# Optimization experiments

Hardware: AMD Instinct MI355X
Metric: run time of the kernel (lower is better)

## Reference

```python
import jax, jax.numpy as jnp
import numpy as np

EPS = 1e-5

def layer_norm(x, g, b):
    mu = jnp.mean(x, axis=-1, keepdims=True)
    var = jnp.mean(jnp.square(x - mu), axis=-1, keepdims=True)
    return (x - mu) * jax.lax.rsqrt(var + EPS) * g + b

def setup_inputs() -> dict:
    key = jax.random.key(0)
    B, N, IN_D, S, D = 64, 4096, 256, 8, 256
    ks = jax.random.split(key, 20)
    scale = lambda fan_in: 1.0 / np.sqrt(fan_in)
    u = lambda k, shape, s: jax.random.uniform(k, shape, jnp.float32, -s, s)
    return {
        "inputs": jax.random.normal(ks[0], (B, N, IN_D), jnp.float32),
        "noise": jax.random.normal(ks[1], (B, S, D), jnp.float32),
        "slots_mu": jax.random.normal(ks[2], (1, S, D), jnp.float32),
        "slots_sigma": jnp.ones((1, S, D), jnp.float32) * 0.1,
        "Wq": u(ks[3], (D, D), scale(D)), "bq": u(ks[4], (D,), scale(D)),
        "Wk": u(ks[5], (D, IN_D), scale(IN_D)), "bk": u(ks[6], (D,), scale(IN_D)),
        "Wv": u(ks[7], (D, IN_D), scale(IN_D)), "bv": u(ks[8], (D,), scale(IN_D)),
        "W_ih": u(ks[9], (3 * D, D), scale(D)), "b_ih": u(ks[10], (3 * D,), scale(D)),
        "W_hh": u(ks[11], (3 * D, D), scale(D)), "b_hh": u(ks[12], (3 * D,), scale(D)),
        "W1": u(ks[13], (D, D), scale(D)), "b1": u(ks[14], (D,), scale(D)),
        "W2": u(ks[15], (D, D), scale(D)), "b2": u(ks[16], (D,), scale(D)),
        "ln_slots_g": jnp.ones((D,), jnp.float32), "ln_slots_b": jnp.zeros((D,), jnp.float32),
        "ln_mlp_g": jnp.ones((D,), jnp.float32), "ln_mlp_b": jnp.zeros((D,), jnp.float32),
    }

def gru_cell(x, h, W_ih, b_ih, W_hh, b_hh):
    # PyTorch GRUCell: gates ordered (reset, update, new)
    gi = x @ W_ih.T + b_ih  # [B*S, 3D]
    gh = h @ W_hh.T + b_hh
    i_r, i_z, i_n = jnp.split(gi, 3, axis=-1)
    h_r, h_z, h_n = jnp.split(gh, 3, axis=-1)
    r = jax.nn.sigmoid(i_r + h_r)
    z = jax.nn.sigmoid(i_z + h_z)
    n = jnp.tanh(i_n + r * h_n)
    return (1.0 - z) * n + z * h

def reference(inputs, noise, slots_mu, slots_sigma, Wq, bq, Wk, bk, Wv, bv,
              W_ih, b_ih, W_hh, b_hh, W1, b1, W2, b2,
              ln_slots_g, ln_slots_b, ln_mlp_g, ln_mlp_b):
    B, N, _ = inputs.shape
    _, S, D = noise.shape
    num_iterations = 3
    slots = slots_mu + slots_sigma * noise  # [B, S, D]
    # k, v are loop-invariant; hoist the big GEMMs out of the iteration loop
    k = jnp.einsum('bnd,ed->bne', inputs, Wk) + bk  # [B, N, D]
    v = jnp.einsum('bnd,ed->bne', inputs, Wv) + bv  # [B, N, D]
    inv_sqrt_d = 1.0 / np.sqrt(D)
    for _ in range(num_iterations):
        slots_prev = slots
        q = layer_norm(slots, ln_slots_g, ln_slots_b) @ Wq.T + bq  # [B, S, D]
        attn_logits = jnp.einsum('bsd,bnd->bsn', q, k) * inv_sqrt_d
        attn = jax.nn.softmax(attn_logits, axis=-1)  # softmax over inputs (dim=-1)
        updates = jnp.einsum('bsn,bnd->bsd', attn, v)  # [B, S, D]
        h_new = gru_cell(updates.reshape(-1, D), slots_prev.reshape(-1, D),
                         W_ih, b_ih, W_hh, b_hh).reshape(B, S, D)
        slots = slots_prev + h_new  # residual around GRU (as in source)
        hidden = jax.nn.relu(layer_norm(slots, ln_mlp_g, ln_mlp_b) @ W1.T + b1)
        slots = slots + (hidden @ W2.T + b2)
    return slots
```

## Files before the change

### kernel.cpp

```cpp
#include <hip/hip_runtime.h>


constexpr int Bn = 64;
constexpr int Nn = 4096;
constexpr int Dd = 256;
constexpr int Ss = 8;
constexpr int CH = 16;
constexpr float EPSF = 1e-5f;

#define DEV __device__ __forceinline__

using short8 = __attribute__((ext_vector_type(8))) short;
using f32x4 = __attribute__((ext_vector_type(4))) float;
union U8 { short8 s; uint4 u; };
union LL { unsigned u[2]; long long l; };

DEV unsigned bfpack2(float lo, float hi) {
  unsigned ul = __float_as_uint(lo), uh = __float_as_uint(hi);
  ul = (ul + 0x7FFFu + ((ul >> 16) & 1u)) >> 16;
  uh = (uh + 0x7FFFu + ((uh >> 16) & 1u)) & 0xFFFF0000u;
  return ul | uh;
}
DEV unsigned short bf16r(float x) {
  unsigned u = __float_as_uint(x);
  u = (u + 0x7FFFu + ((u >> 16) & 1u)) >> 16;
  return (unsigned short)u;
}
DEV unsigned f8q(float x) {
  unsigned u = __float_as_uint(x), s = (u >> 24) & 0x80u;
  float a = __uint_as_float(u & 0x7FFFFFFFu);
  if (a >= 448.f) return s | 0x7Eu;
  if (a < 0.015625f) {
    int m = (int)rintf(a * 512.f);
    return s | (unsigned)m;
  }
  unsigned v = (u & 0x7FFFFFFFu) + 0x7FFFFu + ((u >> 20) & 1u);
  unsigned E = (v >> 23) - 120u;
  unsigned M = (v >> 20) & 7u;
  if (E > 15u) return s | 0x7Eu;
  unsigned r = (E << 3) | M;
  if (r > 0x7Eu) r = 0x7Eu;
  return s | r;
}
DEV float rsum32(float v) {
  v += __shfl_xor(v, 1); v += __shfl_xor(v, 2); v += __shfl_xor(v, 4);
  v += __shfl_xor(v, 8); v += __shfl_xor(v, 16);
  return v;
}
DEV float sigm(float x) { return 1.f / (1.f + __expf(-x)); }

template <int NK>
DEV void load_af(short8* a, const unsigned short* base, int lda, int m16, int quad) {
  const unsigned short* p = base + m16 * lda + quad * 8;
#pragma unroll
  for (int kk = 0; kk < NK; ++kk) a[kk] = *(const short8*)(p + kk * 32);
}
template <int NK>
DEV f32x4 gemm_tile(const short8* a, const unsigned short* wr, float binit) {
  f32x4 acc = {binit, binit, binit, binit};
#pragma unroll
  for (int kk = 0; kk < NK; ++kk) {
    short8 b = *(const short8*)(wr + kk * 32);
    acc = __builtin_amdgcn_mfma_f32_16x16x32_bf16(a[kk], b, acc, 0, 0, 0);
  }
  return acc;
}

DEV void ln_row8(const float* x, const float* g, const float* b, int d0,
                 unsigned short* dst) {
  float s = x[0] + x[1] + x[2] + x[3] + x[4] + x[5] + x[6] + x[7];
  float mu = rsum32(s) * (1.f / 256.f);
  float q = 0.f;
#pragma unroll
  for (int j = 0; j < 8; ++j) { float d = x[j] - mu; q += d * d; }
  float rs = rsqrtf(rsum32(q) * (1.f / 256.f) + EPSF);
  float o[8];
#pragma unroll
  for (int j = 0; j < 8; ++j) o[j] = (x[j] - mu) * rs * g[d0 + j] + b[d0 + j];
  uint4 w;
  w.x = bfpack2(o[0], o[1]); w.y = bfpack2(o[2], o[3]);
  w.z = bfpack2(o[4], o[5]); w.w = bfpack2(o[6], o[7]);
  *(uint4*)dst = w;
}

__global__ __launch_bounds__(256) void k_prep(
    const float* __restrict__ Wq, const float* __restrict__ Wk,
    const float* __restrict__ bq, unsigned short* __restrict__ Wqk_b,
    float* __restrict__ bqk, const float* __restrict__ Wv,
    const float* __restrict__ Wih, const float* __restrict__ Whh,
    const float* __restrict__ W1, const float* __restrict__ W2,
    const float* __restrict__ bih, const float* __restrict__ bhh,
    unsigned* Wv_b, unsigned* Wzr_b, unsigned* Win_b, unsigned* Whn_b,
    unsigned* W1_b, unsigned* W2_b, float* bzr) {
  const int u = blockIdx.x, tid = threadIdx.x;
  if (u < 32) {
    const int c0 = u * 8;
    float acc[8] = {0.f, 0.f, 0.f, 0.f, 0.f, 0.f, 0.f, 0.f};
    for (int e = 0; e < 256; ++e) {
      float wq = Wq[e * 256 + tid];
      const float* wk = Wk + e * 256 + c0;
#pragma unroll
      for (int j = 0; j < 8; ++j) acc[j] += wq * wk[j];
    }
#pragma unroll
    for (int j = 0; j < 8; ++j) Wqk_b[(c0 + j) * 256 + tid] = bf16r(acc[j]);
  } else if (u == 32) {
    float acc = 0.f;
    for (int e = 0; e < 256; ++e) acc += bq[e] * Wk[e * 256 + tid];
    bqk[tid] = acc;
  } else {
    int cu = u - 33;
    if (cu >= 1152) {
      int i = (cu - 1152) * 256 + tid;
      if (i < 512) bzr[i] = bih[i] + bhh[i];
      return;
    }
    int p = cu * 256 + tid;
    const float* src; unsigned* dst;
    if (p < 32768) { src = Wv + 2 * p; dst = Wv_b + p; }
    else if (p < 163840) {
      int q = p - 32768, row = q >> 8, col = (q & 255) * 2;
      src = (col < 256) ? (Wih + row * 256 + col) : (Whh + row * 256 + col - 256);
      dst = Wzr_b + q;
    }
    else if (p < 196608) { int q = p - 163840; src = Wih + 512 * 256 + 2 * q; dst = Win_b + q; }
    else if (p < 229376) { int q = p - 196608; src = Whh + 512 * 256 + 2 * q; dst = Whn_b + q; }
    else if (p < 262144) { int q = p - 229376; src = W1 + 2 * q; dst = W1_b + q; }
    else { int q = p - 262144; src = W2 + 2 * q; dst = W2_b + q; }
    dst[0] = bfpack2(src[0], src[1]);
  }
}

__global__ __launch_bounds__(256) void k_xconv(const float* __restrict__ xin,
                                               unsigned char* __restrict__ xbf) {
#pragma unroll
  for (int j = 0; j < 4; ++j) {
    int flat = blockIdx.x * 1024 + j * 256 + threadIdx.x;
    const float4* src = (const float4*)(xin + (size_t)flat * 8);
    float4 v0 = src[0], v1 = src[1];
    uint2 o;
    o.x = f8q(v0.x) | (f8q(v0.y) << 8) | (f8q(v0.z) << 16) | (f8q(v0.w) << 24);
    o.y = f8q(v1.x) | (f8q(v1.y) << 8) | (f8q(v1.z) << 16) | (f8q(v1.w) << 24);
    ((uint2*)xbf)[flat] = o;
  }
}

__global__ __launch_bounds__(512) void k_qk0(const float* __restrict__ noise,
                                             const float* __restrict__ s_mu,
                                             const float* __restrict__ s_sg,
                                             const float* __restrict__ gsl,
                                             const float* __restrict__ bsl,
                                             const unsigned short* __restrict__ Wqk_b,
                                             const float* __restrict__ bqk,
                                             float* __restrict__ slots,
                                             float* __restrict__ qk) {
  __shared__ __align__(16) unsigned short lnb[16 * 264];
  const int tid = threadIdx.x, bb = blockIdx.x;
  const int lane = tid & 63, wave = tid >> 6;
  const int m16 = lane & 15, quad = lane >> 4;
  const int row = tid >> 5, l32 = tid & 31, d0 = l32 * 8;
  {
    const int grow = bb * 16 + row;
    const int sidx = (grow & 7) * 256 + d0;
    const float* np = noise + (size_t)grow * 256 + d0;
    float4 n0 = *(const float4*)np, n1 = *(const float4*)(np + 4);
    float4 m0 = *(const float4*)(s_mu + sidx), m1 = *(const float4*)(s_mu + sidx + 4);
    float4 g0 = *(const float4*)(s_sg + sidx), g1 = *(const float4*)(s_sg + sidx + 4);
    float x[8] = {m0.x + g0.x * n0.x, m0.y + g0.y * n0.y,
                  m0.z + g0.z * n0.z, m0.w + g0.w * n0.w,
                  m1.x + g1.x * n1.x, m1.y + g1.y * n1.y,
                  m1.z + g1.z * n1.z, m1.w + g1.w * n1.w};
    float* sp_ = slots + (size_t)grow * 256 + d0;
    float4 o0, o1;
    o0.x = x[0]; o0.y = x[1]; o0.z = x[2]; o0.w = x[3];
    o1.x = x[4]; o1.y = x[5]; o1.z = x[6]; o1.w = x[7];
    *(float4*)sp_ = o0; *(float4*)(sp_ + 4) = o1;
    ln_row8(x, gsl, bsl, d0, lnb + row * 264 + d0);
  }
  __syncthreads();
  short8 a8[8];
  load_af<8>(a8, lnb, 264, m16, quad);
#pragma unroll
  for (int i = 0; i < 2; ++i) {
    int t = wave + 8 * i;
    f32x4 acc = gemm_tile<8>(a8, Wqk_b + (size_t)(t * 16 + m16) * 256 + quad * 8,
                             bqk[t * 16 + m16]);
#pragma unroll
    for (int r = 0; r < 4; ++r)
      qk[(size_t)(bb * 16 + quad * 4 + r) * 256 + t * 16 + m16] = acc[r];
  }
}

__global__ __launch_bounds__(256) void k_attn(const unsigned char* __restrict__ xbf,
                                              const float* __restrict__ qk,
                                              float* __restrict__ pl,
                                              float* __restrict__ pu) {
  __shared__ __align__(16) unsigned xr[64 * 68];
  __shared__ __align__(16) unsigned xt[64 * 68];
  __shared__ __align__(16) unsigned char pp[16 * 72];
  __shared__ __align__(16) float lred[4][16];
  const int tid = threadIdx.x;
  const int lane = tid & 63, wave = tid >> 6;
  const int m16 = lane & 15, quad = lane >> 4;
  const int c = blockIdx.x, b = blockIdx.y;
  const int pb = (b * CH + c) * 8;
  const size_t row0 = (size_t)b * Nn + (size_t)c * 256;

  LL aq[8];
  {
    const float* qrow = qk + (size_t)(b * 8 + (m16 & 7)) * 256 + quad * 8;
#pragma unroll
    for (int kk = 0; kk < 8; ++kk) {
      float4 q0 = *(const float4*)(qrow + kk * 32);
      float4 q1 = *(const float4*)(qrow + kk * 32 + 4);
      unsigned lo = f8q(q0.x) | (f8q(q0.y) << 8) | (f8q(q0.z) << 16) | (f8q(q0.w) << 24);
      unsigned hi = f8q(q1.x) | (f8q(q1.y) << 8) | (f8q(q1.z) << 16) | (f8q(q1.w) << 24);
      if (m16 >= 8) { lo = 0u; hi = 0u; }
      aq[kk].u[0] = lo; aq[kk].u[1] = hi;
    }
  }
  float lacc[4] = {0.f, 0.f, 0.f, 0.f};
  f32x4 acc[4];
#pragma unroll
  for (int t = 0; t < 4; ++t) acc[t] = (f32x4){0.f, 0.f, 0.f, 0.f};
  const int d0w = wave * 64;

  const uint4* xb4 = (const uint4*)xbf;
  uint4 pr[4];
#pragma unroll
  for (int i = 0; i < 4; ++i) {
    int flat = i * 256 + tid, n = flat >> 4, od = flat & 15;
    pr[i] = xb4[(row0 + n) * 16 + od];
  }

  for (int ch = 0; ch < 4; ++ch) {
#pragma unroll
    for (int i = 0; i < 4; ++i) {
      int flat = i * 256 + tid, n = flat >> 4, od = flat & 15;
      *(uint4*)(xr + n * 68 + od * 4) = pr[i];
      xt[(od * 4 + 0) * 68 + n] = pr[i].x;
      xt[(od * 4 + 1) * 68 + n] = pr[i].y;
      xt[(od * 4 + 2) * 68 + n] = pr[i].z;
      xt[(od * 4 + 3) * 68 + n] = pr[i].w;
    }
    __syncthreads();
    if (ch + 1 < 4) {
      const size_t nb = row0 + (size_t)(ch + 1) * 64;
#pragma unroll
      for (int i = 0; i < 4; ++i) {
        int flat = i * 256 + tid, n = flat >> 4, od = flat & 15;
        pr[i] = xb4[(nb + n) * 16 + od];
      }
    }
    {
      const int nt = wave;
      f32x4 pacc = (f32x4){0.f, 0.f, 0.f, 0.f};
      const unsigned* xrr = xr + (nt * 16 + m16) * 68 + quad * 2;
#pragma unroll
      for (int kk = 0; kk < 8; ++kk) {
        LL bf;
        bf.l = *(const long long*)(xrr + kk * 8);
        pacc = __builtin_amdgcn_mfma_f32_16x16x32_fp8_fp8(aq[kk].l, bf.l, pacc, 0, 0, 0);
      }
      const int n = nt * 16 + m16;
#pragma unroll
      for (int r = 0; r < 4; ++r) {
        float p = __expf(pacc[r] * 0.0625f);
        lacc[r] += p;
        pp[(quad * 4 + r) * 72 + n] = (unsigned char)f8q(p);
      }
    }
    __syncthreads();
    const unsigned bsel = (m16 & 3) | (((m16 & 3) + 4) << 8);
#pragma unroll
    for (int nh = 0; nh < 2; ++nh) {
      LL bp;
      bp.l = *(const long long*)(pp + m16 * 72 + nh * 32 + quad * 8);
#pragma unroll
      for (int t = 0; t < 4; ++t) {
        int dq = (d0w + t * 16 + m16) >> 2;
        const unsigned* xtp = xt + dq * 68 + nh * 32 + quad * 8;
        uint4 w0 = *(const uint4*)xtp;
        uint4 w1 = *(const uint4*)(xtp + 4);
        unsigned e0 = __builtin_amdgcn_perm(w0.y, w0.x, bsel);
        unsigned e1 = __builtin_amdgcn_perm(w0.w, w0.z, bsel);
        unsigned e2 = __builtin_amdgcn_perm(w1.y, w1.x, bsel);
        unsigned e3 = __builtin_amdgcn_perm(w1.w, w1.z, bsel);
        LL af;
        af.u[0] = __builtin_amdgcn_perm(e1, e0, 0x05040100u);
        af.u[1] = __builtin_amdgcn_perm(e3, e2, 0x05040100u);
        acc[t] = __builtin_amdgcn_mfma_f32_16x16x32_fp8_fp8(af.l, bp.l, acc[t], 0, 0, 0);
      }
    }
    __syncthreads();
  }
  if (m16 < 8) {
#pragma unroll
    for (int t = 0; t < 4; ++t)
#pragma unroll
      for (int r = 0; r < 4; ++r)
        pu[(size_t)(pb + m16) * 256 + d0w + t * 16 + quad * 4 + r] = acc[t][r];
  }
#pragma unroll
  for (int r = 0; r < 4; ++r) {
    float v = lacc[r];
    v += __shfl_xor(v, 1); v += __shfl_xor(v, 2);
    v += __shfl_xor(v, 4); v += __shfl_xor(v, 8);
    if (m16 == 0) lred[wave][quad * 4 + r] = v;
  }
  __syncthreads();
  if (tid < 8)
    pl[pb + tid] = lred[0][tid] + lred[1][tid] + lred[2][tid] + lred[3][tid];
}

__global__ __launch_bounds__(512) void k_upd(
    const float* __restrict__ pl, const float* __restrict__ pu,
    const unsigned short* __restrict__ Wv_b, const float* __restrict__ bv,
    const unsigned short* __restrict__ Wzr_b, const float* __restrict__ bzr,
    const unsigned short* __restrict__ Win_b, const float* __restrict__ bin,
    const unsigned short* __restrict__ Whn_b, const float* __restrict__ bhn,
    const unsigned short* __restrict__ W1_b, const float* __restrict__ b1,
    const unsigned short* __restrict__ W2_b, const float* __restrict__ b2,
    const float* __restrict__ gml, const float* __restrict__ bml,
    const float* __restrict__ gsl, const float* __restrict__ bsl,
    const unsigned short* __restrict__ Wqk_b, const float* __restrict__ bqk,
    float* __restrict__ slots, float* __restrict__ qk, float* __restrict__ dout) {
  __shared__ __align__(16) unsigned short cat[16 * 520];
  __shared__ __align__(16) float sp[16 * 260];
  __shared__ __align__(16) float s1[16 * 260];
  __shared__ __align__(16) unsigned short lnb[16 * 264];
  const int tid = threadIdx.x, bb = blockIdx.x;
  const int lane = tid & 63, wave = tid >> 6;
  const int m16 = lane & 15, quad = lane >> 4;
  const int row = tid >> 5, l32 = tid & 31, d0 = l32 * 8;
  const int bat = 2 * bb + (row >> 3), sl = row & 7;
  {
    float L = 0.f;
#pragma unroll
    for (int cc = 0; cc < 16; ++cc) L += pl[(bat * 16 + cc) * 8 + sl];
    float li = 1.f / L;
    float a[8] = {0.f, 0.f, 0.f, 0.f, 0.f, 0.f, 0.f, 0.f};
    for (int cc = 0; cc < 16; ++cc) {
      const float* pp_ = pu + ((size_t)(bat * 16 + cc) * 8 + sl) * 256 + d0;
      float4 v0 = *(const float4*)pp_, v1 = *(const float4*)(pp_ + 4);
      a[0] += v0.x; a[1] += v0.y; a[2] += v0.z; a[3] += v0.w;
      a[4] += v1.x; a[5] += v1.y; a[6] += v1.z; a[7] += v1.w;
    }
    uint4 o;
    o.x = bfpack2(a[0] * li, a[1] * li); o.y = bfpack2(a[2] * li, a[3] * li);
    o.z = bfpack2(a[4] * li, a[5] * li); o.w = bfpack2(a[6] * li, a[7] * li);
    *(uint4*)(cat + row * 520 + d0) = o;
    const float* sp_ = slots + (size_t)(bb * 16 + row) * 256 + d0;
    float4 h0 = *(const float4*)sp_, h1 = *(const float4*)(sp_ + 4);
    *(float4*)(sp + row * 260 + d0) = h0;
    *(float4*)(sp + row * 260 + d0 + 4) = h1;
    uint4 hb;
    hb.x = bfpack2(h0.x, h0.y); hb.y = bfpack2(h0.z, h0.w);
    hb.z = bfpack2(h1.x, h1.y); hb.w = bfpack2(h1.z, h1.w);
    *(uint4*)(cat + row * 520 + 256 + d0) = hb;
  }
  __syncthreads();
  short8 afr[16];
  load_af<8>(afr, cat, 520, m16, quad);
  f32x4 accv[2];
#pragma unroll
  for (int i = 0; i < 2; ++i) {
    int t = wave + 8 * i;
    accv[i] = gemm_tile<8>(afr, Wv_b + (size_t)(t * 16 + m16) * 256 + quad * 8,
                           bv[t * 16 + m16]);
  }
  __syncthreads();
#pragma unroll
  for (int i = 0; i < 2; ++i) {
    int t = wave + 8 * i;
#pragma unroll
    for (int r = 0; r < 4; ++r)
      cat[(quad * 4 + r) * 520 + t * 16 + m16] = bf16r(accv[i][r]);
  }
  __syncthreads();
  load_af<16>(afr, cat, 520, m16, quad);
  f32x4 rr[2], zz[2];
#pragma unroll
  for (int i = 0; i < 2; ++i) {
    int t = wave + 8 * i;
    f32x4 ar = gemm_tile<16>(afr, Wzr_b + (size_t)(t * 16 + m16) * 512 + quad * 8,
                             bzr[t * 16 + m16]);
    f32x4 az = gemm_tile<16>(afr, Wzr_b + (size_t)((t + 16) * 16 + m16) * 512 + quad * 8,
                             bzr[(t + 16) * 16 + m16]);
#pragma unroll
    for (int r = 0; r < 4; ++r) { rr[i][r] = sigm(ar[r]); zz[i][r] = sigm(az[r]); }
  }
#pragma unroll
  for (int i = 0; i < 2; ++i) {
    int t = wave + 8 * i, col = t * 16 + m16;
    f32x4 ain = gemm_tile<8>(afr, Win_b + (size_t)(t * 16 + m16) * 256 + quad * 8,
                             bin[col]);
    f32x4 ahn = gemm_tile<8>(afr + 8, Whn_b + (size_t)(t * 16 + m16) * 256 + quad * 8,
                             bhn[col]);
#pragma unroll
    for (int r = 0; r < 4; ++r) {
      int rw = quad * 4 + r;
      float nin = ain[r] + rr[i][r] * ahn[r];
      float nn = 1.f - 2.f / (__expf(2.f * nin) + 1.f);
      float hpc = sp[rw * 260 + col];
      s1[rw * 260 + col] = hpc + (1.f - zz[i][r]) * nn + zz[i][r] * hpc;
    }
  }
  __syncthreads();
  {
    const float* s1r = s1 + row * 260 + d0;
    float4 v0 = *(const float4*)s1r, v1 = *(const float4*)(s1r + 4);
    float x[8] = {v0.x, v0.y, v0.z, v0.w, v1.x, v1.y, v1.z, v1.w};
    ln_row8(x, gml, bml, d0, lnb + row * 264 + d0);
  }
  __syncthreads();
  load_af<8>(afr, lnb, 264, m16, quad);
#pragma unroll
  for (int i = 0; i < 2; ++i) {
    int t = wave + 8 * i;
    f32x4 acc = gemm_tile<8>(afr, W1_b + (size_t)(t * 16 + m16) * 256 + quad * 8,
                             b1[t * 16 + m16]);
#pragma unroll
    for (int r = 0; r < 4; ++r)
      cat[(quad * 4 + r) * 520 + t * 16 + m16] = bf16r(fmaxf(acc[r], 0.f));
  }
  __syncthreads();
  load_af<8>(afr, cat, 520, m16, quad);
#pragma unroll
  for (int i = 0; i < 2; ++i) {
    int t = wave + 8 * i;
    f32x4 acc = gemm_tile<8>(afr, W2_b + (size_t)(t * 16 + m16) * 256 + quad * 8,
                             b2[t * 16 + m16]);
#pragma unroll
    for (int r = 0; r < 4; ++r) {
      int rw = quad * 4 + r, col = t * 16 + m16;
      float v = acc[r] + s1[rw * 260 + col];
      size_t gi = (size_t)(bb * 16 + rw) * 256 + col;
      slots[gi] = v;
      if (dout) dout[gi] = v;
      sp[rw * 260 + col] = v;
    }
  }
  __syncthreads();
  {
    const float* spr = sp + row * 260 + d0;
    float4 v0 = *(const float4*)spr, v1 = *(const float4*)(spr + 4);
    float x[8] = {v0.x, v0.y, v0.z, v0.w, v1.x, v1.y, v1.z, v1.w};
    ln_row8(x, gsl, bsl, d0, lnb + row * 264 + d0);
  }
  __syncthreads();
  load_af<8>(afr, lnb, 264, m16, quad);
#pragma unroll
  for (int i = 0; i < 2; ++i) {
    int t = wave + 8 * i;
    f32x4 acc = gemm_tile<8>(afr, Wqk_b + (size_t)(t * 16 + m16) * 256 + quad * 8,
                             bqk[t * 16 + m16]);
#pragma unroll
    for (int r = 0; r < 4; ++r)
      qk[(size_t)(bb * 16 + quad * 4 + r) * 256 + t * 16 + m16] = acc[r];
  }
}

extern "C" void kernel_launch(void* const* d_in, const int* in_sizes, int n_in,
                              void* d_out, int out_size, void* d_ws, size_t ws_size,
                              hipStream_t stream) {
  const float* inputs = (const float*)d_in[0];
  const float* noise = (const float*)d_in[1];
  const float* s_mu = (const float*)d_in[2];
  const float* s_sg = (const float*)d_in[3];
  const float* Wq = (const float*)d_in[4];
  const float* bq = (const float*)d_in[5];
  const float* Wk = (const float*)d_in[6];
  const float* Wv = (const float*)d_in[8];
  const float* bv = (const float*)d_in[9];
  const float* Wih = (const float*)d_in[10];
  const float* bih = (const float*)d_in[11];
  const float* Whh = (const float*)d_in[12];
  const float* bhh = (const float*)d_in[13];
  const float* W1 = (const float*)d_in[14];
  const float* b1 = (const float*)d_in[15];
  const float* W2 = (const float*)d_in[16];
  const float* b2 = (const float*)d_in[17];
  const float* gsl = (const float*)d_in[18];
  const float* bsl = (const float*)d_in[19];
  const float* gml = (const float*)d_in[20];
  const float* bml = (const float*)d_in[21];
  float* out = (float*)d_out;

  char* wsb = (char*)d_ws;
  unsigned char* xbf = (unsigned char*)wsb;
  float* fp = (float*)(wsb + (size_t)Bn * Nn * Dd * 2);
  float* slots = fp; fp += Bn * Ss * Dd;
  float* qk = fp;    fp += Bn * Ss * Dd;
  float* bqk = fp;   fp += Dd;
  float* pl = fp;    fp += Bn * CH * Ss;
  float* pu = fp;    fp += Bn * CH * Ss * Dd;
  float* bzr = fp;   fp += 512;
  unsigned short* wb = (unsigned short*)fp;
  unsigned short* Wv_b = wb;  wb += 65536;
  unsigned short* Wzr_b = wb; wb += 262144;
  unsigned short* Win_b = wb; wb += 65536;
  unsigned short* Whn_b = wb; wb += 65536;
  unsigned short* W1_b = wb;  wb += 65536;
  unsigned short* W2_b = wb;  wb += 65536;
  unsigned short* Wqk_b = wb; wb += 65536;
  (void)in_sizes; (void)n_in; (void)out_size; (void)ws_size;

  k_xconv<<<dim3(8192), dim3(256), 0, stream>>>(inputs, xbf);
  k_prep<<<dim3(1187), dim3(256), 0, stream>>>(
      Wq, Wk, bq, Wqk_b, bqk, Wv, Wih, Whh, W1, W2, bih, bhh, (unsigned*)Wv_b,
      (unsigned*)Wzr_b, (unsigned*)Win_b, (unsigned*)Whn_b, (unsigned*)W1_b,
      (unsigned*)W2_b, bzr);
  k_qk0<<<dim3(32), dim3(512), 0, stream>>>(noise, s_mu, s_sg, gsl, bsl, Wqk_b, bqk,
                                            slots, qk);
  for (int it = 0; it < 3; ++it) {
    k_attn<<<dim3(CH, Bn), dim3(256), 0, stream>>>(xbf, qk, pl, pu);
    k_upd<<<dim3(32), dim3(512), 0, stream>>>(
        pl, pu, Wv_b, bv, Wzr_b, bzr, Win_b, bih + 512, Whn_b, bhh + 512, W1_b, b1,
        W2_b, b2, gml, bml, gsl, bsl, Wqk_b, bqk, slots, qk, (it == 2) ? out : nullptr);
  }
}
```

Measured before the change: 678.1 us.

## Split attention into logits and aggregation kernels, fuse fp8 input conversion, atomic reductions

Fuses the fp32-to-fp8 input conversion into the first iteration's logits kernel, so the separate conversion pass no longer re-reads the inputs. Attention is split into kernel A, which computes exp(logits) into a global fp8 probability buffer with atomically accumulated denominators, and kernel B, which aggregates values with double-buffered LDS and atomically adds into a per-iteration update buffer. The cross-chunk reduction leaves k_upd, and q is stored as fp8 directly. This adds a global round trip for the probabilities, float atomics (nondeterministic order), and zero-initialisation of the accumulation buffers in the prep kernel.

```diff
diff --git a/kernel.cpp b/kernel.cpp
--- a/kernel.cpp
+++ b/kernel.cpp
@@ -91,7 +91,7 @@
     const float* __restrict__ W1, const float* __restrict__ W2,
     const float* __restrict__ bih, const float* __restrict__ bhh,
     unsigned* Wv_b, unsigned* Wzr_b, unsigned* Win_b, unsigned* Whn_b,
-    unsigned* W1_b, unsigned* W2_b, float* bzr) {
+    unsigned* W1_b, unsigned* W2_b, float* bzr, float* zbuf) {
   const int u = blockIdx.x, tid = threadIdx.x;
   if (u < 32) {
     const int c0 = u * 8;
@@ -108,14 +108,8 @@
     float acc = 0.f;
     for (int e = 0; e < 256; ++e) acc += bq[e] * Wk[e * 256 + tid];
     bqk[tid] = acc;
-  } else {
-    int cu = u - 33;
-    if (cu >= 1152) {
-      int i = (cu - 1152) * 256 + tid;
-      if (i < 512) bzr[i] = bih[i] + bhh[i];
-      return;
-    }
-    int p = cu * 256 + tid;
+  } else if (u < 1185) {
+    int p = (u - 33) * 256 + tid;
     const float* src; unsigned* dst;
     if (p < 32768) { src = Wv + 2 * p; dst = Wv_b + p; }
     else if (p < 163840) {
@@ -128,20 +122,12 @@
     else if (p < 262144) { int q = p - 229376; src = W1 + 2 * q; dst = W1_b + q; }
     else { int q = p - 262144; src = W2 + 2 * q; dst = W2_b + q; }
     dst[0] = bfpack2(src[0], src[1]);
-  }
-}
-
-__global__ __launch_bounds__(256) void k_xconv(const float* __restrict__ xin,
-                                               unsigned char* __restrict__ xbf) {
-#pragma unroll
-  for (int j = 0; j < 4; ++j) {
-    int flat = blockIdx.x * 1024 + j * 256 + threadIdx.x;
-    const float4* src = (const float4*)(xin + (size_t)flat * 8);
-    float4 v0 = src[0], v1 = src[1];
-    uint2 o;
-    o.x = f8q(v0.x) | (f8q(v0.y) << 8) | (f8q(v0.z) << 16) | (f8q(v0.w) << 24);
-    o.y = f8q(v1.x) | (f8q(v1.y) << 8) | (f8q(v1.z) << 16) | (f8q(v1.w) << 24);
-    ((uint2*)xbf)[flat] = o;
+  } else if (u < 1187) {
+    int i = (u - 1185) * 256 + tid;
+    if (i < 512) bzr[i] = bih[i] + bhh[i];
+  } else {
+    int idx = (u - 1187) * 256 + tid;
+    if (idx < 98688) ((float4*)zbuf)[idx] = make_float4(0.f, 0.f, 0.f, 0.f);
   }
 }
 
@@ -153,7 +139,7 @@
                                              const unsigned short* __restrict__ Wqk_b,
                                              const float* __restrict__ bqk,
                                              float* __restrict__ slots,
-                                             float* __restrict__ qk) {
+                                             unsigned char* __restrict__ qk8) {
   __shared__ __align__(16) unsigned short lnb[16 * 264];
   const int tid = threadIdx.x, bb = blockIdx.x;
   const int lane = tid & 63, wave = tid >> 6;
@@ -187,99 +173,120 @@
                              bqk[t * 16 + m16]);
 #pragma unroll
     for (int r = 0; r < 4; ++r)
-      qk[(size_t)(bb * 16 + quad * 4 + r) * 256 + t * 16 + m16] = acc[r];
-  }
-}
-
-__global__ __launch_bounds__(256) void k_attn(const unsigned char* __restrict__ xbf,
-                                              const float* __restrict__ qk,
-                                              float* __restrict__ pl,
-                                              float* __restrict__ pu) {
-  __shared__ __align__(16) unsigned xr[64 * 68];
-  __shared__ __align__(16) unsigned xt[64 * 68];
-  __shared__ __align__(16) unsigned char pp[16 * 72];
-  __shared__ __align__(16) float lred[4][16];
-  const int tid = threadIdx.x;
-  const int lane = tid & 63, wave = tid >> 6;
+      qk8[(size_t)(bb * 16 + quad * 4 + r) * 256 + t * 16 + m16] =
+          (unsigned char)f8q(acc[r]);
+  }
+}
+
+template <bool FIRST>
+__global__ __launch_bounds__(256) void k_attnA(const float* __restrict__ xin,
+                                               unsigned char* __restrict__ xbf,
+                                               const unsigned char* __restrict__ q8,
+                                               unsigned char* __restrict__ ppg,
+                                               float* __restrict__ plf) {
+  const int tid = threadIdx.x, lane = tid & 63, wave = tid >> 6;
+  const int m16 = lane & 15, quad = lane >> 4;
+  const int c64 = blockIdx.x, b = blockIdx.y;
+  const size_t grow = (size_t)b * Nn + c64 * 64 + wave * 16 + m16;
+  LL aq[8];
+  {
+    const unsigned char* qrow = q8 + ((size_t)b * 8 + (m16 & 7)) * 256 + quad * 8;
+#pragma unroll
+    for (int kk = 0; kk < 8; ++kk) {
+      long long v = *(const long long*)(qrow + kk * 32);
+      aq[kk].l = (m16 >= 8) ? 0ll : v;
+    }
+  }
+  f32x4 pacc = (f32x4){0.f, 0.f, 0.f, 0.f};
+  if (FIRST) {
+    const float* xr = xin + grow * 256 + quad * 8;
+    unsigned char* xw = xbf + grow * 256 + quad * 8;
+#pragma unroll
+    for (int kk = 0; kk < 8; ++kk) {
+      float4 v0 = *(const float4*)(xr + kk * 32);
+      float4 v1 = *(const float4*)(xr + kk * 32 + 4);
+      LL bf;
+      bf.u[0] = f8q(v0.x) | (f8q(v0.y) << 8) | (f8q(v0.z) << 16) | (f8q(v0.w) << 24);
+      bf.u[1] = f8q(v1.x) | (f8q(v1.y) << 8) | (f8q(v1.z) << 16) | (f8q(v1.w) << 24);
+      *(uint2*)(xw + kk * 32) = make_uint2(bf.u[0], bf.u[1]);
+      pacc = __builtin_amdgcn_mfma_f32_16x16x32_fp8_fp8(aq[kk].l, bf.l, pacc, 0, 0, 0);
+    }
+  } else {
+    const unsigned char* xr = xbf + grow * 256 + quad * 8;
+#pragma unroll
+    for (int kk = 0; kk < 8; ++kk) {
+      LL bf;
+      bf.l = *(const long long*)(xr + kk * 32);
+      pacc = __builtin_amdgcn_mfma_f32_16x16x32_fp8_fp8(aq[kk].l, bf.l, pacc, 0, 0, 0);
+    }
+  }
+  const int u = b * CH + (c64 >> 2);
+  const int nloc = (c64 & 3) * 64 + wave * 16 + m16;
+  float lacc[4];
+#pragma unroll
+  for (int r = 0; r < 4; ++r) {
+    float p = __expf(pacc[r] * 0.0625f);
+    lacc[r] = p;
+    if (quad < 2)
+      ppg[((size_t)u * 8 + quad * 4 + r) * 256 + nloc] = (unsigned char)f8q(p);
+  }
+#pragma unroll
+  for (int r = 0; r < 4; ++r) {
+    float v = lacc[r];
+    v += __shfl_xor(v, 1); v += __shfl_xor(v, 2);
+    v += __shfl_xor(v, 4); v += __shfl_xor(v, 8);
+    if (m16 == 0 && quad < 2) atomicAdd(&plf[b * 8 + quad * 4 + r], v);
+  }
+}
+
+__global__ __launch_bounds__(256) void k_attnB(const unsigned char* __restrict__ xbf,
+                                               const unsigned char* __restrict__ ppg,
+                                               float* __restrict__ ua) {
+  __shared__ __align__(16) unsigned xt[2][64 * 68];
+  const int tid = threadIdx.x, lane = tid & 63, wave = tid >> 6;
   const int m16 = lane & 15, quad = lane >> 4;
   const int c = blockIdx.x, b = blockIdx.y;
-  const int pb = (b * CH + c) * 8;
+  const int u = b * CH + c;
   const size_t row0 = (size_t)b * Nn + (size_t)c * 256;
-
-  LL aq[8];
+  const unsigned bsel = (m16 & 3) | (((m16 & 3) + 4) << 8);
+  LL bp[8];
   {
-    const float* qrow = qk + (size_t)(b * 8 + (m16 & 7)) * 256 + quad * 8;
-#pragma unroll
-    for (int kk = 0; kk < 8; ++kk) {
-      float4 q0 = *(const float4*)(qrow + kk * 32);
-      float4 q1 = *(const float4*)(qrow + kk * 32 + 4);
-      unsigned lo = f8q(q0.x) | (f8q(q0.y) << 8) | (f8q(q0.z) << 16) | (f8q(q0.w) << 24);
-      unsigned hi = f8q(q1.x) | (f8q(q1.y) << 8) | (f8q(q1.z) << 16) | (f8q(q1.w) << 24);
-      if (m16 >= 8) { lo = 0u; hi = 0u; }
-      aq[kk].u[0] = lo; aq[kk].u[1] = hi;
-    }
-  }
-  float lacc[4] = {0.f, 0.f, 0.f, 0.f};
+    const unsigned char* bpp = ppg + (size_t)u * 2048 + (m16 & 7) * 256 + quad * 8;
+#pragma unroll
+    for (int k8 = 0; k8 < 8; ++k8) {
+      long long v = *(const long long*)(bpp + k8 * 32);
+      bp[k8].l = (m16 >= 8) ? 0ll : v;
+    }
+  }
   f32x4 acc[4];
 #pragma unroll
   for (int t = 0; t < 4; ++t) acc[t] = (f32x4){0.f, 0.f, 0.f, 0.f};
-  const int d0w = wave * 64;
-
-  const uint4* xb4 = (const uint4*)xbf;
+  const uint4* xb4 = (const uint4*)(xbf + row0 * 256);
   uint4 pr[4];
 #pragma unroll
-  for (int i = 0; i < 4; ++i) {
-    int flat = i * 256 + tid, n = flat >> 4, od = flat & 15;
-    pr[i] = xb4[(row0 + n) * 16 + od];
-  }
+  for (int i = 0; i < 4; ++i) pr[i] = xb4[i * 256 + tid];
 
   for (int ch = 0; ch < 4; ++ch) {
+    unsigned* xtb = xt[ch & 1];
 #pragma unroll
     for (int i = 0; i < 4; ++i) {
       int flat = i * 256 + tid, n = flat >> 4, od = flat & 15;
-      *(uint4*)(xr + n * 68 + od * 4) = pr[i];
-      xt[(od * 4 + 0) * 68 + n] = pr[i].x;
-      xt[(od * 4 + 1) * 68 + n] = pr[i].y;
-      xt[(od * 4 + 2) * 68 + n] = pr[i].z;
-      xt[(od * 4 + 3) * 68 + n] = pr[i].w;
+      xtb[(od * 4 + 0) * 68 + n] = pr[i].x;
+      xtb[(od * 4 + 1) * 68 + n] = pr[i].y;
+      xtb[(od * 4 + 2) * 68 + n] = pr[i].z;
+      xtb[(od * 4 + 3) * 68 + n] = pr[i].w;
     }
     __syncthreads();
     if (ch + 1 < 4) {
-      const size_t nb = row0 + (size_t)(ch + 1) * 64;
-#pragma unroll
-      for (int i = 0; i < 4; ++i) {
-        int flat = i * 256 + tid, n = flat >> 4, od = flat & 15;
-        pr[i] = xb4[(nb + n) * 16 + od];
-      }
-    }
-    {
-      const int nt = wave;
-      f32x4 pacc = (f32x4){0.f, 0.f, 0.f, 0.f};
-      const unsigned* xrr = xr + (nt * 16 + m16) * 68 + quad * 2;
-#pragma unroll
-      for (int kk = 0; kk < 8; ++kk) {
-        LL bf;
-        bf.l = *(const long long*)(xrr + kk * 8);
-        pacc = __builtin_amdgcn_mfma_f32_16x16x32_fp8_fp8(aq[kk].l, bf.l, pacc, 0, 0, 0);
-      }
-      const int n = nt * 16 + m16;
-#pragma unroll
-      for (int r = 0; r < 4; ++r) {
-        float p = __expf(pacc[r] * 0.0625f);
-        lacc[r] += p;
-        pp[(quad * 4 + r) * 72 + n] = (unsigned char)f8q(p);
-      }
-    }
-    __syncthreads();
-    const unsigned bsel = (m16 & 3) | (((m16 & 3) + 4) << 8);
+#pragma unroll
+      for (int i = 0; i < 4; ++i) pr[i] = xb4[(ch + 1) * 1024 + i * 256 + tid];
+    }
 #pragma unroll
     for (int nh = 0; nh < 2; ++nh) {
-      LL bp;
-      bp.l = *(const long long*)(pp + m16 * 72 + nh * 32 + quad * 8);
 #pragma unroll
       for (int t = 0; t < 4; ++t) {
-        int dq = (d0w + t * 16 + m16) >> 2;
-        const unsigned* xtp = xt + dq * 68 + nh * 32 + quad * 8;
+        int dq = wave * 16 + t * 4 + (m16 >> 2);
+        const unsigned* xtp = xtb + dq * 68 + nh * 32 + quad * 8;
         uint4 w0 = *(const uint4*)xtp;
         uint4 w1 = *(const uint4*)(xtp + 4);
         unsigned e0 = __builtin_amdgcn_perm(w0.y, w0.x, bsel);
@@ -289,32 +296,24 @@
         LL af;
         af.u[0] = __builtin_amdgcn_perm(e1, e0, 0x05040100u);
         af.u[1] = __builtin_amdgcn_perm(e3, e2, 0x05040100u);
-        acc[t] = __builtin_amdgcn_mfma_f32_16x16x32_fp8_fp8(af.l, bp.l, acc[t], 0, 0, 0);
+        acc[t] = __builtin_amdgcn_mfma_f32_16x16x32_fp8_fp8(af.l, bp[ch * 2 + nh].l,
+                                                            acc[t], 0, 0, 0);
       }
     }
-    __syncthreads();
   }
   if (m16 < 8) {
+    const int d0w = wave * 64;
 #pragma unroll
     for (int t = 0; t < 4; ++t)
 #pragma unroll
       for (int r = 0; r < 4; ++r)
-        pu[(size_t)(pb + m16) * 256 + d0w + t * 16 + quad * 4 + r] = acc[t][r];
-  }
-#pragma unroll
-  for (int r = 0; r < 4; ++r) {
-    float v = lacc[r];
-    v += __shfl_xor(v, 1); v += __shfl_xor(v, 2);
-    v += __shfl_xor(v, 4); v += __shfl_xor(v, 8);
-    if (m16 == 0) lred[wave][quad * 4 + r] = v;
-  }
-  __syncthreads();
-  if (tid < 8)
-    pl[pb + tid] = lred[0][tid] + lred[1][tid] + lred[2][tid] + lred[3][tid];
+        atomicAdd(&ua[((size_t)b * 8 + m16) * 256 + d0w + t * 16 + quad * 4 + r],
+                  acc[t][r]);
+  }
 }
 
 __global__ __launch_bounds__(512) void k_upd(
-    const float* __restrict__ pl, const float* __restrict__ pu,
+    const float* __restrict__ plf, const float* __restrict__ ua,
     const unsigned short* __restrict__ Wv_b, const float* __restrict__ bv,
     const unsigned short* __restrict__ Wzr_b, const float* __restrict__ bzr,
     const unsigned short* __restrict__ Win_b, const float* __restrict__ bin,
@@ -324,7 +323,8 @@
     const float* __restrict__ gml, const float* __restrict__ bml,
     const float* __restrict__ gsl, const float* __restrict__ bsl,
     const unsigned short* __restrict__ Wqk_b, const float* __restrict__ bqk,
-    float* __restrict__ slots, float* __restrict__ qk, float* __restrict__ dout) {
+    float* __restrict__ slots, unsigned char* __restrict__ qk8,
+    float* __restrict__ dout) {
   __shared__ __align__(16) unsigned short cat[16 * 520];
   __shared__ __align__(16) float sp[16 * 260];
   __shared__ __align__(16) float s1[16 * 260];
@@ -335,20 +335,12 @@
   const int row = tid >> 5, l32 = tid & 31, d0 = l32 * 8;
   const int bat = 2 * bb + (row >> 3), sl = row & 7;
   {
-    float L = 0.f;
-#pragma unroll
-    for (int cc = 0; cc < 16; ++cc) L += pl[(bat * 16 + cc) * 8 + sl];
-    float li = 1.f / L;
-    float a[8] = {0.f, 0.f, 0.f, 0.f, 0.f, 0.f, 0.f, 0.f};
-    for (int cc = 0; cc < 16; ++cc) {
-      const float* pp_ = pu + ((size_t)(bat * 16 + cc) * 8 + sl) * 256 + d0;
-      float4 v0 = *(const float4*)pp_, v1 = *(const float4*)(pp_ + 4);
-      a[0] += v0.x; a[1] += v0.y; a[2] += v0.z; a[3] += v0.w;
-      a[4] += v1.x; a[5] += v1.y; a[6] += v1.z; a[7] += v1.w;
-    }
+    float li = 1.f / plf[bat * 8 + sl];
+    const float* up = ua + ((size_t)(bat * 8 + sl)) * 256 + d0;
+    float4 a0 = *(const float4*)up, a1 = *(const float4*)(up + 4);
     uint4 o;
-    o.x = bfpack2(a[0] * li, a[1] * li); o.y = bfpack2(a[2] * li, a[3] * li);
-    o.z = bfpack2(a[4] * li, a[5] * li); o.w = bfpack2(a[6] * li, a[7] * li);
+    o.x = bfpack2(a0.x * li, a0.y * li); o.y = bfpack2(a0.z * li, a0.w * li);
+    o.z = bfpack2(a1.x * li, a1.y * li); o.w = bfpack2(a1.z * li, a1.w * li);
     *(uint4*)(cat + row * 520 + d0) = o;
     const float* sp_ = slots + (size_t)(bb * 16 + row) * 256 + d0;
     float4 h0 = *(const float4*)sp_, h1 = *(const float4*)(sp_ + 4);
@@ -457,7 +449,8 @@
                              bqk[t * 16 + m16]);
 #pragma unroll
     for (int r = 0; r < 4; ++r)
-      qk[(size_t)(bb * 16 + quad * 4 + r) * 256 + t * 16 + m16] = acc[r];
+      qk8[(size_t)(bb * 16 + quad * 4 + r) * 256 + t * 16 + m16] =
+          (unsigned char)f8q(acc[r]);
   }
 }
 
@@ -489,13 +482,15 @@
 
   char* wsb = (char*)d_ws;
   unsigned char* xbf = (unsigned char*)wsb;
-  float* fp = (float*)(wsb + (size_t)Bn * Nn * Dd * 2);
+  unsigned char* q8 = (unsigned char*)(wsb + ((size_t)Bn * Nn * Dd * 2));
+  unsigned char* ppg = q8 + (size_t)Bn * Ss * Dd;
+  float* fp = (float*)(ppg + (size_t)Bn * CH * Ss * 256);
   float* slots = fp; fp += Bn * Ss * Dd;
-  float* qk = fp;    fp += Bn * Ss * Dd;
   float* bqk = fp;   fp += Dd;
-  float* pl = fp;    fp += Bn * CH * Ss;
-  float* pu = fp;    fp += Bn * CH * Ss * Dd;
   float* bzr = fp;   fp += 512;
+  float* zbuf = fp;
+  float* pl3 = fp;   fp += 3 * 512;
+  float* ua3 = fp;   fp += 3 * Bn * Ss * Dd;
   unsigned short* wb = (unsigned short*)fp;
   unsigned short* Wv_b = wb;  wb += 65536;
   unsigned short* Wzr_b = wb; wb += 262144;
@@ -506,17 +501,22 @@
   unsigned short* Wqk_b = wb; wb += 65536;
   (void)in_sizes; (void)n_in; (void)out_size; (void)ws_size;
 
-  k_xconv<<<dim3(8192), dim3(256), 0, stream>>>(inputs, xbf);
-  k_prep<<<dim3(1187), dim3(256), 0, stream>>>(
+  k_prep<<<dim3(1573), dim3(256), 0, stream>>>(
       Wq, Wk, bq, Wqk_b, bqk, Wv, Wih, Whh, W1, W2, bih, bhh, (unsigned*)Wv_b,
       (unsigned*)Wzr_b, (unsigned*)Win_b, (unsigned*)Whn_b, (unsigned*)W1_b,
-      (unsigned*)W2_b, bzr);
+      (unsigned*)W2_b, bzr, zbuf);
   k_qk0<<<dim3(32), dim3(512), 0, stream>>>(noise, s_mu, s_sg, gsl, bsl, Wqk_b, bqk,
-                                            slots, qk);
+                                            slots, q8);
   for (int it = 0; it < 3; ++it) {
-    k_attn<<<dim3(CH, Bn), dim3(256), 0, stream>>>(xbf, qk, pl, pu);
+    float* plf = pl3 + it * 512;
+    float* ua = ua3 + (size_t)it * Bn * Ss * Dd;
+    if (it == 0)
+      k_attnA<true><<<dim3(64, 64), dim3(256), 0, stream>>>(inputs, xbf, q8, ppg, plf);
+    else
+      k_attnA<false><<<dim3(64, 64), dim3(256), 0, stream>>>(inputs, xbf, q8, ppg, plf);
+    k_attnB<<<dim3(CH, Bn), dim3(256), 0, stream>>>(xbf, ppg, ua);
     k_upd<<<dim3(32), dim3(512), 0, stream>>>(
-        pl, pu, Wv_b, bv, Wzr_b, bzr, Win_b, bih + 512, Whn_b, bhh + 512, W1_b, b1,
-        W2_b, b2, gml, bml, gsl, bsl, Wqk_b, bqk, slots, qk, (it == 2) ? out : nullptr);
-  }
-}
+        plf, ua, Wv_b, bv, Wzr_b, bzr, Win_b, bih + 512, Whn_b, bhh + 512, W1_b, b1,
+        W2_b, b2, gml, bml, gsl, bsl, Wqk_b, bqk, slots, q8, (it == 2) ? out : nullptr);
+  }
+}
```

Result: slower. 1.051 ms (+55.0%).
